# Kernel optimization log

Hardware: AMD Instinct MI355X
Metric: run time of the kernel (lower is better)

The kernel has to match this reference:

```python
import jax, jax.numpy as jnp
import numpy as np
from jax import lax

H = 32  # hidden size


def _lstm_layer(x, Wih, Whh, bih, bhh):
    """x: [B, T, D_in]; returns [B, T, H]. PyTorch gate order i,f,g,o."""
    B = x.shape[0]
    b = bih + bhh  # [4H]
    # precompute input projections for all timesteps: [T, B, 4H]
    xp = jnp.einsum('btd,gd->tbg', x, Wih) + b

    def step(carry, xt):
        h, c = carry
        gates = xt + h @ Whh.T  # [B, 4H]
        i, f, g, o = jnp.split(gates, 4, axis=-1)
        i = jax.nn.sigmoid(i)
        f = jax.nn.sigmoid(f)
        g = jnp.tanh(g)
        o = jax.nn.sigmoid(o)
        c = f * c + i * g
        h = o * jnp.tanh(c)
        return (h, c), h

    init = (jnp.zeros((B, H), x.dtype), jnp.zeros((B, H), x.dtype))
    _, ys = lax.scan(step, init, xp)  # ys: [T, B, H]
    return jnp.swapaxes(ys, 0, 1)


def _lstm5(x, Wih0, Wih_rest, Whh, bih, bhh):
    h = _lstm_layer(x, Wih0, Whh[0], bih[0], bhh[0])
    for l in range(4):  # fixed small layer count
        h = _lstm_layer(h, Wih_rest[l], Whh[l + 1], bih[l + 1], bhh[l + 1])
    return h


def setup_inputs() -> dict:
    key = jax.random.key(0)
    ks = jax.random.split(key, 18)
    s = 1.0 / np.sqrt(H)
    B, T = 16384, 20
    u = lambda k, shp: jax.random.uniform(k, shp, jnp.float32, -s, s)
    return {
        'accel': jax.random.normal(ks[0], (B, T, 3), jnp.float32),
        'gyro': jax.random.normal(ks[1], (B, T, 3), jnp.float32),
        'accel_Wih0': u(ks[2], (4 * H, 3)),
        'accel_Wih_rest': u(ks[3], (4, 4 * H, H)),
        'accel_Whh': u(ks[4], (5, 4 * H, H)),
        'accel_bih': u(ks[5], (5, 4 * H)),
        'accel_bhh': u(ks[6], (5, 4 * H)),
        'gyro_Wih0': u(ks[7], (4 * H, 3)),
        'gyro_Wih_rest': u(ks[8], (4, 4 * H, H)),
        'gyro_Whh': u(ks[9], (5, 4 * H, H)),
        'gyro_bih': u(ks[10], (5, 4 * H)),
        'gyro_bhh': u(ks[11], (5, 4 * H)),
        'fc1_w': u(ks[12], (128, T * H * 2)),
        'fc1_b': u(ks[13], (128,)),
        'fc2_w': u(ks[14], (5, 128)),
        'fc2_b': u(ks[15], (5,)),
    }


def reference(accel, gyro, accel_Wih0, accel_Wih_rest, accel_Whh, accel_bih,
              accel_bhh, gyro_Wih0, gyro_Wih_rest, gyro_Whh, gyro_bih,
              gyro_bhh, fc1_w, fc1_b, fc2_w, fc2_b):
    a = _lstm5(accel, accel_Wih0, accel_Wih_rest, accel_Whh, accel_bih, accel_bhh)
    g = _lstm5(gyro, gyro_Wih0, gyro_Wih_rest, gyro_Whh, gyro_bih, gyro_bhh)
    x = jnp.concatenate([a, g], axis=1)          # [B, 2T, H]
    x = x.reshape(x.shape[0], -1)                # [B, 2*T*H]
    x = jax.nn.relu(x @ fc1_w.T + fc1_b)         # [B, 128]
    return x @ fc2_w.T + fc2_b                   # [B, 5]
```

## Files before the change

kernel.cpp:

```cpp
#include <hip/hip_runtime.h>
#include <math.h>

#define B_TOTAL 16384
#define T_STEPS 20
#define NGRP    1024

typedef __attribute__((ext_vector_type(8))) __bf16 bf16x8;
typedef __attribute__((ext_vector_type(4))) float f32x4;

#define LOG2E_F 1.4426950408889634f
#define K2_F    2.8853900817779268f

__device__ __forceinline__ float exp2_fast(float x) {
#if __has_builtin(__builtin_amdgcn_exp2f)
    return __builtin_amdgcn_exp2f(x);
#else
    return __expf(x * 0.6931471805599453f);
#endif
}

__device__ __forceinline__ __bf16 bf16_bits(unsigned short s) {
    __bf16 r; __builtin_memcpy(&r, &s, 2); return r;
}
__device__ __forceinline__ void split_trunc(float x, __bf16& hi, __bf16& lo) {
    unsigned u = __float_as_uint(x);
    hi = bf16_bits((unsigned short)(u >> 16));
    float l = x - __uint_as_float(u & 0xFFFF0000u);
    lo = bf16_bits((unsigned short)(__float_as_uint(l) >> 16));
}

__device__ __forceinline__ float lstm_act2(f32x4 a, float& c) {
    float eA = exp2_fast(-a[0]);
    float eB = exp2_fast(-a[1]);
    float eC = exp2_fast(a[2]);
    float aA = 1.0f + eA, aB = 1.0f + eB, aC = 1.0f + eC;
    float pAC = aA * aC;
    float r1  = __builtin_amdgcn_rcpf(pAC * aB);
    c = fmaf(c, pAC, (eC - 1.0f) * aB) * r1;
    float eD = exp2_fast(-a[3]);
    float eE = exp2_fast(K2_F * c);
    float r2 = __builtin_amdgcn_rcpf((1.0f + eD) * (1.0f + eE));
    return (eE - 1.0f) * r2;
}

__global__ __launch_bounds__(512, 8)
void lstm5_mfma(const float* __restrict__ accel, const float* __restrict__ gyro,
                const float* __restrict__ aWih0, const float* __restrict__ aWihR,
                const float* __restrict__ aWhh,  const float* __restrict__ aBih,
                const float* __restrict__ aBhh,
                const float* __restrict__ gWih0, const float* __restrict__ gWihR,
                const float* __restrict__ gWhh,  const float* __restrict__ gBih,
                const float* __restrict__ gBhh,
                __bf16* __restrict__ Xhi, __bf16* __restrict__ Xlo) {
    const int tid  = threadIdx.x;
    const int w    = tid >> 6;
    const int lane = tid & 63;
    const int e    = lane & 15;
    const int quad = lane >> 4;
    const int sensor = blockIdx.y;
    const int bbase  = blockIdx.x * 16;

    const float* xin  = sensor ? gyro  : accel;
    const float* Wih0 = sensor ? gWih0 : aWih0;
    const float* WihR = sensor ? gWihR : aWihR;
    const float* Whh  = sensor ? gWhh  : aWhh;
    const float* Bih  = sensor ? gBih  : aBih;
    const float* Bhh  = sensor ? gBhh  : aBhh;

    __shared__ __align__(16) __bf16 shi[T_STEPS * 512];
    __shared__ __align__(16) __bf16 slo[T_STEPS * 512];

    const int ug  = w * 4 + quad;
    const int swz = (e >> 1) & 3;

    const int widx = (e * 16 + ((w * 2 + (quad >> 1)) ^ (swz << 2))) * 2 + (quad & 1);
    const int rb_base = e * 32 + ((quad ^ swz) << 3);

    const int m_row = lane & 15;
    const int orow  = (m_row & 3) * 32 + (w * 4 + (m_row >> 2));
    const float wscale = ((m_row & 3) == 2) ? K2_F : LOG2E_F;

    bf16x8 wih_h, wih_l, whh_h, whh_l;
    bf16x8 ih_h, ih_l;
    f32x4  biasv;
    float  c0 = 0.f;

#define LOAD_FRAG(Wsrc, fh, fl)                               \
    {                                                         \
        const float* p_ = (Wsrc) + (orow) * 32 + quad * 8;    \
        _Pragma("unroll")                                     \
        for (int jj = 0; jj < 8; ++jj) {                      \
            __bf16 h_, l_;                                    \
            split_trunc(p_[jj] * wscale, h_, l_);             \
            (fh)[jj] = h_;  (fl)[jj] = l_;                    \
        }                                                     \
    }

#define LOAD_BIAS(l)                                                        \
    {                                                                       \
        _Pragma("unroll")                                                   \
        for (int r = 0; r < 4; ++r) {                                       \
            float bs_ = (r == 2) ? K2_F : LOG2E_F;                          \
            biasv[r] = (Bih[(l) * 128 + r * 32 + ug] +                      \
                        Bhh[(l) * 128 + r * 32 + ug]) * bs_;                \
        }                                                                   \
    }

    {
        LOAD_FRAG(Whh, whh_h, whh_l);
        LOAD_BIAS(0);
        float w0reg[4][3];
#pragma unroll
        for (int r = 0; r < 4; ++r) {
            float bs_ = (r == 2) ? K2_F : LOG2E_F;
#pragma unroll
            for (int k = 0; k < 3; ++k)
                w0reg[r][k] = Wih0[(r * 32 + ug) * 3 + k] * bs_;
        }
        const float* xrow = xin + (size_t)(bbase + e) * (T_STEPS * 3);

        for (int t = 0; t < T_STEPS; ++t) {
            float x0 = xrow[t * 3 + 0];
            float x1 = xrow[t * 3 + 1];
            float x2 = xrow[t * 3 + 2];
            f32x4 acc = biasv;
#pragma unroll
            for (int r = 0; r < 4; ++r)
                acc[r] = fmaf(w0reg[r][0], x0,
                         fmaf(w0reg[r][1], x1,
                         fmaf(w0reg[r][2], x2, acc[r])));
            if (t > 0) {
                int rb = (t - 1) * 512 + rb_base;
                bf16x8 bh = *(const bf16x8*)&shi[rb];
                bf16x8 bl = *(const bf16x8*)&slo[rb];
                acc = __builtin_amdgcn_mfma_f32_16x16x32_bf16(whh_h, bh, acc, 0, 0, 0);
                acc = __builtin_amdgcn_mfma_f32_16x16x32_bf16(whh_h, bl, acc, 0, 0, 0);
                acc = __builtin_amdgcn_mfma_f32_16x16x32_bf16(whh_l, bh, acc, 0, 0, 0);
            }
            float h0 = lstm_act2(acc, c0);
            __bf16 hh_, ll_;
            split_trunc(h0, hh_, ll_);
            shi[t * 512 + widx] = hh_;
            slo[t * 512 + widx] = ll_;
            __syncthreads();
        }
    }

#define STEP_L(t)                                                           \
    {                                                                       \
        bf16x8 bh, bl, pf_h, pf_l;                                          \
        if ((t) > 0) {                                                      \
            bh = *(const bf16x8*)&shi[((t) - 1) * 512 + rb_base];           \
            bl = *(const bf16x8*)&slo[((t) - 1) * 512 + rb_base];           \
        }                                                                   \
        if ((t) < T_STEPS - 1) {               \
            pf_h = *(const bf16x8*)&shi[((t) + 1) * 512 + rb_base];         \
            pf_l = *(const bf16x8*)&slo[((t) + 1) * 512 + rb_base];         \
        }                                                                   \
        f32x4 acc;                                                          \
        acc = __builtin_amdgcn_mfma_f32_16x16x32_bf16(wih_h, ih_h, biasv, 0, 0, 0); \
        acc = __builtin_amdgcn_mfma_f32_16x16x32_bf16(wih_h, ih_l, acc, 0, 0, 0);   \
        acc = __builtin_amdgcn_mfma_f32_16x16x32_bf16(wih_l, ih_h, acc, 0, 0, 0);   \
        if ((t) > 0) {                                                      \
            acc = __builtin_amdgcn_mfma_f32_16x16x32_bf16(whh_h, bh, acc, 0, 0, 0); \
            acc = __builtin_amdgcn_mfma_f32_16x16x32_bf16(whh_h, bl, acc, 0, 0, 0); \
            acc = __builtin_amdgcn_mfma_f32_16x16x32_bf16(whh_l, bh, acc, 0, 0, 0); \
        }                                                                   \
        float h0 = lstm_act2(acc, c0);                                      \
        __bf16 hh_, ll_;                                                    \
        split_trunc(h0, hh_, ll_);                                          \
        shi[(t) * 512 + widx] = hh_;                                        \
        slo[(t) * 512 + widx] = ll_;                                        \
        if ((t) < T_STEPS - 1) { ih_h = pf_h; ih_l = pf_l; }                \
        __syncthreads();                 \
    }

    for (int l = 1; l < 5; ++l) {
        const float* Wi = WihR + (l - 1) * 4096;
        const float* Wh = Whh + l * 4096;
        LOAD_FRAG(Wi, wih_h, wih_l);
        LOAD_FRAG(Wh, whh_h, whh_l);
        LOAD_BIAS(l);
        c0 = 0.f;

        ih_h = *(const bf16x8*)&shi[rb_base];
        ih_l = *(const bf16x8*)&slo[rb_base];
        __syncthreads();

#pragma unroll
        for (int t = 0; t < T_STEPS; ++t) STEP_L(t);
    }
    __syncthreads();

    {
        size_t base = ((size_t)(sensor * NGRP + blockIdx.x)) * (20 * 512);
        float4* dh = (float4*)(Xhi + base);
        float4* dl = (float4*)(Xlo + base);
        const float4* sh = (const float4*)shi;
        const float4* sl = (const float4*)slo;
        for (int i = tid; i < 1280; i += 512) { dh[i] = sh[i]; dl[i] = sl[i]; }
    }
#undef LOAD_FRAG
#undef LOAD_BIAS
#undef STEP_L
}

__global__ void w1_prep(const float* __restrict__ w1,
                        __bf16* __restrict__ w1ah, __bf16* __restrict__ w1al) {
    int t = blockIdx.x * blockDim.x + threadIdx.x;
    if (t >= 20480) return;
    int lane = t & 63;
    int ks   = (t >> 6) % 40;
    int mt   = t / (64 * 40);
    int row  = mt * 16 + (lane & 15);
    int col0 = ks * 32 + (lane >> 4) * 8;
    const float* src = w1 + row * 1280 + col0;
#pragma unroll
    for (int j = 0; j < 8; ++j) {
        __bf16 h_, l_;
        split_trunc(src[j], h_, l_);
        w1ah[t * 8 + j] = h_;
        w1al[t * 8 + j] = l_;
    }
}

__global__ __launch_bounds__(256, 4)
void fc_mfma(const __bf16* __restrict__ Xhi, const __bf16* __restrict__ Xlo,
             const __bf16* __restrict__ w1ah, const __bf16* __restrict__ w1al,
             const float* __restrict__ fc1_b, const float* __restrict__ fc2_w,
             const float* __restrict__ fc2_b, float* __restrict__ out) {
    const int tid  = threadIdx.x;
    const int wv   = tid >> 6;
    const int lane = tid & 63;
    const int e    = lane & 15;
    const int quad = lane >> 4;
    const int g    = blockIdx.x;

    const int lnoff = e * 32 + ((quad ^ ((e >> 1) & 3)) << 3);

    __shared__ __align__(16) f32x4 sacc[4][8][64];
    __shared__ float sred[4][16][5];

    f32x4 acc[8];
#pragma unroll
    for (int m = 0; m < 8; ++m) acc[m] = (f32x4){0.f, 0.f, 0.f, 0.f};

    for (int kk = 0; kk < 10; ++kk) {
        int ks = wv * 10 + kk;
        int sensor = ks / 20, t = ks % 20;
        size_t bb = ((size_t)(sensor * NGRP + g)) * (20 * 512) + t * 512 + lnoff;
        bf16x8 bh = *(const bf16x8*)(Xhi + bb);
        bf16x8 bl = *(const bf16x8*)(Xlo + bb);
#pragma unroll
        for (int m = 0; m < 8; ++m) {
            const __bf16* ap = w1ah + ((size_t)((m * 40 + ks) * 64 + lane)) * 8;
            const __bf16* al = w1al + ((size_t)((m * 40 + ks) * 64 + lane)) * 8;
            bf16x8 ah = *(const bf16x8*)ap;
            bf16x8 av = *(const bf16x8*)al;
            acc[m] = __builtin_amdgcn_mfma_f32_16x16x32_bf16(ah, bh, acc[m], 0, 0, 0);
            acc[m] = __builtin_amdgcn_mfma_f32_16x16x32_bf16(ah, bl, acc[m], 0, 0, 0);
            acc[m] = __builtin_amdgcn_mfma_f32_16x16x32_bf16(av, bh, acc[m], 0, 0, 0);
        }
    }
#pragma unroll
    for (int m = 0; m < 8; ++m) sacc[wv][m][lane] = acc[m];
    __syncthreads();

    float p[5] = {0.f, 0.f, 0.f, 0.f, 0.f};
#pragma unroll
    for (int mm = 0; mm < 2; ++mm) {
        int mt = wv * 2 + mm;
        f32x4 z = sacc[0][mt][lane];
#pragma unroll
        for (int k = 1; k < 4; ++k) {
            f32x4 zz = sacc[k][mt][lane];
#pragma unroll
            for (int r = 0; r < 4; ++r) z[r] += zz[r];
        }
#pragma unroll
        for (int r = 0; r < 4; ++r) {
            int row = mt * 16 + quad * 4 + r;
            float v = fmaxf(z[r] + fc1_b[row], 0.f);
#pragma unroll
            for (int n = 0; n < 5; ++n) p[n] = fmaf(v, fc2_w[n * 128 + row], p[n]);
        }
    }
#pragma unroll
    for (int n = 0; n < 5; ++n) {
        p[n] += __shfl_xor(p[n], 16, 64);
        p[n] += __shfl_xor(p[n], 32, 64);
    }
    if (quad == 0) {
#pragma unroll
        for (int n = 0; n < 5; ++n) sred[wv][e][n] = p[n];
    }
    __syncthreads();
    if (tid < 80) {
        int col = tid / 5, n = tid - col * 5;
        out[(size_t)(g * 16 + col) * 5 + n] =
            sred[0][col][n] + sred[1][col][n] + sred[2][col][n] + sred[3][col][n] + fc2_b[n];
    }
}

extern "C" void kernel_launch(void* const* d_in, const int* in_sizes, int n_in,
                              void* d_out, int out_size, void* d_ws, size_t ws_size,
                              hipStream_t stream) {
    const float* accel  = (const float*)d_in[0];
    const float* gyro   = (const float*)d_in[1];
    const float* aWih0  = (const float*)d_in[2];
    const float* aWihR  = (const float*)d_in[3];
    const float* aWhh   = (const float*)d_in[4];
    const float* aBih   = (const float*)d_in[5];
    const float* aBhh   = (const float*)d_in[6];
    const float* gWih0  = (const float*)d_in[7];
    const float* gWihR  = (const float*)d_in[8];
    const float* gWhh   = (const float*)d_in[9];
    const float* gBih   = (const float*)d_in[10];
    const float* gBhh   = (const float*)d_in[11];
    const float* fc1_w  = (const float*)d_in[12];
    const float* fc1_b  = (const float*)d_in[13];
    const float* fc2_w  = (const float*)d_in[14];
    const float* fc2_b  = (const float*)d_in[15];
    float* out = (float*)d_out;

    const size_t XN = (size_t)2 * NGRP * 20 * 512;
    __bf16* Xhi  = (__bf16*)d_ws;
    __bf16* Xlo  = Xhi + XN;
    __bf16* W1ah = Xlo + XN;
    __bf16* W1al = W1ah + 163840;

    hipLaunchKernelGGL(w1_prep, dim3(80), dim3(256), 0, stream, fc1_w, W1ah, W1al);

    hipLaunchKernelGGL(lstm5_mfma, dim3(NGRP, 2), dim3(512), 0, stream,
                       accel, gyro, aWih0, aWihR, aWhh, aBih, aBhh,
                       gWih0, gWihR, gWhh, gBih, gBhh, Xhi, Xlo);

    hipLaunchKernelGGL(fc_mfma, dim3(NGRP), dim3(256), 0, stream,
                       Xhi, Xlo, W1ah, W1al, fc1_b, fc2_w, fc2_b, out);
}
```

Baseline: 285.7 us.

## Fuse fc1 GEMM into LSTM kernel epilogue, emit per-sensor partial sums

The LSTM kernel now runs the fc1 matmul directly from its shared-memory hidden states. Each wave computes one 16-row tile of the 128 outputs over its sensor's 20 timesteps and writes fp32 partial sums. This removes the round trip through global memory of the bf16 hi/lo hidden-state buffers, and a small reduce kernel now adds the two sensor partials and applies ReLU and fc2. In exchange, the LSTM kernel does extra MFMA work and global weight loads in its tail, and the removed __syncthreads before the shared-memory reads needs the last step to already be synchronised.

```diff
diff --git a/kernel.cpp b/kernel.cpp
--- a/kernel.cpp
+++ b/kernel.cpp
@@ -51,7 +51,8 @@
                 const float* __restrict__ gWih0, const float* __restrict__ gWihR,
                 const float* __restrict__ gWhh,  const float* __restrict__ gBih,
                 const float* __restrict__ gBhh,
-                __bf16* __restrict__ Xhi, __bf16* __restrict__ Xlo) {
+                const __bf16* __restrict__ w1ah, const __bf16* __restrict__ w1al,
+                float* __restrict__ partial) {
     const int tid  = threadIdx.x;
     const int w    = tid >> 6;
     const int lane = tid & 63;
@@ -190,15 +191,25 @@
 #pragma unroll
         for (int t = 0; t < T_STEPS; ++t) STEP_L(t);
     }
-    __syncthreads();
 
     {
-        size_t base = ((size_t)(sensor * NGRP + blockIdx.x)) * (20 * 512);
-        float4* dh = (float4*)(Xhi + base);
-        float4* dl = (float4*)(Xlo + base);
-        const float4* sh = (const float4*)shi;
-        const float4* sl = (const float4*)slo;
-        for (int i = tid; i < 1280; i += 512) { dh[i] = sh[i]; dl[i] = sl[i]; }
+        const __bf16* Wh1 = w1ah + ((size_t)(w * 40 + sensor * 20) * 64 + lane) * 8;
+        const __bf16* Wl1 = w1al + ((size_t)(w * 40 + sensor * 20) * 64 + lane) * 8;
+        f32x4 acc = (f32x4){0.f, 0.f, 0.f, 0.f};
+#pragma unroll
+        for (int t = 0; t < T_STEPS; ++t) {
+            bf16x8 bh = *(const bf16x8*)&shi[t * 512 + rb_base];
+            bf16x8 bl = *(const bf16x8*)&slo[t * 512 + rb_base];
+            bf16x8 ah = *(const bf16x8*)(Wh1 + (size_t)t * 512);
+            bf16x8 av = *(const bf16x8*)(Wl1 + (size_t)t * 512);
+            acc = __builtin_amdgcn_mfma_f32_16x16x32_bf16(ah, bh, acc, 0, 0, 0);
+            acc = __builtin_amdgcn_mfma_f32_16x16x32_bf16(ah, bl, acc, 0, 0, 0);
+            acc = __builtin_amdgcn_mfma_f32_16x16x32_bf16(av, bh, acc, 0, 0, 0);
+        }
+        float4 v = make_float4(acc[0], acc[1], acc[2], acc[3]);
+        *(float4*)(partial +
+                   ((size_t)(sensor * NGRP + blockIdx.x) * 8 + w) * 256 +
+                   e * 16 + quad * 4) = v;
     }
 #undef LOAD_FRAG
 #undef LOAD_BIAS
@@ -225,80 +236,46 @@
 }
 
 __global__ __launch_bounds__(256, 4)
-void fc_mfma(const __bf16* __restrict__ Xhi, const __bf16* __restrict__ Xlo,
-             const __bf16* __restrict__ w1ah, const __bf16* __restrict__ w1al,
-             const float* __restrict__ fc1_b, const float* __restrict__ fc2_w,
-             const float* __restrict__ fc2_b, float* __restrict__ out) {
-    const int tid  = threadIdx.x;
-    const int wv   = tid >> 6;
-    const int lane = tid & 63;
-    const int e    = lane & 15;
-    const int quad = lane >> 4;
-    const int g    = blockIdx.x;
-
-    const int lnoff = e * 32 + ((quad ^ ((e >> 1) & 3)) << 3);
-
-    __shared__ __align__(16) f32x4 sacc[4][8][64];
-    __shared__ float sred[4][16][5];
-
-    f32x4 acc[8];
-#pragma unroll
-    for (int m = 0; m < 8; ++m) acc[m] = (f32x4){0.f, 0.f, 0.f, 0.f};
-
-    for (int kk = 0; kk < 10; ++kk) {
-        int ks = wv * 10 + kk;
-        int sensor = ks / 20, t = ks % 20;
-        size_t bb = ((size_t)(sensor * NGRP + g)) * (20 * 512) + t * 512 + lnoff;
-        bf16x8 bh = *(const bf16x8*)(Xhi + bb);
-        bf16x8 bl = *(const bf16x8*)(Xlo + bb);
-#pragma unroll
-        for (int m = 0; m < 8; ++m) {
-            const __bf16* ap = w1ah + ((size_t)((m * 40 + ks) * 64 + lane)) * 8;
-            const __bf16* al = w1al + ((size_t)((m * 40 + ks) * 64 + lane)) * 8;
-            bf16x8 ah = *(const bf16x8*)ap;
-            bf16x8 av = *(const bf16x8*)al;
-            acc[m] = __builtin_amdgcn_mfma_f32_16x16x32_bf16(ah, bh, acc[m], 0, 0, 0);
-            acc[m] = __builtin_amdgcn_mfma_f32_16x16x32_bf16(ah, bl, acc[m], 0, 0, 0);
-            acc[m] = __builtin_amdgcn_mfma_f32_16x16x32_bf16(av, bh, acc[m], 0, 0, 0);
-        }
-    }
-#pragma unroll
-    for (int m = 0; m < 8; ++m) sacc[wv][m][lane] = acc[m];
-    __syncthreads();
+void fc2_reduce(const float* __restrict__ partial,
+                const float* __restrict__ fc1_b, const float* __restrict__ fc2_w,
+                const float* __restrict__ fc2_b, float* __restrict__ out) {
+    const int tid = threadIdx.x;
+    const int col = tid >> 4;
+    const int rg  = tid & 15;
+    const int g   = blockIdx.x;
+
+    const int row0 = rg * 8;
+    const int mt   = row0 >> 4;
+    const int rl0  = row0 & 15;
+    const float* pa = partial + ((size_t)g * 8 + mt) * 256 + col * 16 + rl0;
+    const float* pb = partial + ((size_t)(NGRP + g) * 8 + mt) * 256 + col * 16 + rl0;
+
+    float4 a0 = *(const float4*)(pa);
+    float4 a1 = *(const float4*)(pa + 4);
+    float4 b0 = *(const float4*)(pb);
+    float4 b1 = *(const float4*)(pb + 4);
+    float z[8] = {a0.x + b0.x, a0.y + b0.y, a0.z + b0.z, a0.w + b0.w,
+                  a1.x + b1.x, a1.y + b1.y, a1.z + b1.z, a1.w + b1.w};
 
     float p[5] = {0.f, 0.f, 0.f, 0.f, 0.f};
 #pragma unroll
-    for (int mm = 0; mm < 2; ++mm) {
-        int mt = wv * 2 + mm;
-        f32x4 z = sacc[0][mt][lane];
-#pragma unroll
-        for (int k = 1; k < 4; ++k) {
-            f32x4 zz = sacc[k][mt][lane];
-#pragma unroll
-            for (int r = 0; r < 4; ++r) z[r] += zz[r];
-        }
-#pragma unroll
-        for (int r = 0; r < 4; ++r) {
-            int row = mt * 16 + quad * 4 + r;
-            float v = fmaxf(z[r] + fc1_b[row], 0.f);
-#pragma unroll
-            for (int n = 0; n < 5; ++n) p[n] = fmaf(v, fc2_w[n * 128 + row], p[n]);
-        }
+    for (int rr = 0; rr < 8; ++rr) {
+        int row = row0 + rr;
+        float v = fmaxf(z[rr] + fc1_b[row], 0.f);
+#pragma unroll
+        for (int n = 0; n < 5; ++n) p[n] = fmaf(v, fc2_w[n * 128 + row], p[n]);
     }
 #pragma unroll
     for (int n = 0; n < 5; ++n) {
-        p[n] += __shfl_xor(p[n], 16, 64);
-        p[n] += __shfl_xor(p[n], 32, 64);
-    }
-    if (quad == 0) {
-#pragma unroll
-        for (int n = 0; n < 5; ++n) sred[wv][e][n] = p[n];
-    }
-    __syncthreads();
-    if (tid < 80) {
-        int col = tid / 5, n = tid - col * 5;
-        out[(size_t)(g * 16 + col) * 5 + n] =
-            sred[0][col][n] + sred[1][col][n] + sred[2][col][n] + sred[3][col][n] + fc2_b[n];
+        p[n] += __shfl_xor(p[n], 1, 64);
+        p[n] += __shfl_xor(p[n], 2, 64);
+        p[n] += __shfl_xor(p[n], 4, 64);
+        p[n] += __shfl_xor(p[n], 8, 64);
+    }
+    if (rg == 0) {
+#pragma unroll
+        for (int n = 0; n < 5; ++n)
+            out[((size_t)g * 16 + col) * 5 + n] = p[n] + fc2_b[n];
     }
 }
 
@@ -323,18 +300,16 @@
     const float* fc2_b  = (const float*)d_in[15];
     float* out = (float*)d_out;
 
-    const size_t XN = (size_t)2 * NGRP * 20 * 512;
-    __bf16* Xhi  = (__bf16*)d_ws;
-    __bf16* Xlo  = Xhi + XN;
-    __bf16* W1ah = Xlo + XN;
+    __bf16* W1ah = (__bf16*)d_ws;
     __bf16* W1al = W1ah + 163840;
+    float*  Pacc = (float*)(W1al + 163840);
 
     hipLaunchKernelGGL(w1_prep, dim3(80), dim3(256), 0, stream, fc1_w, W1ah, W1al);
 
     hipLaunchKernelGGL(lstm5_mfma, dim3(NGRP, 2), dim3(512), 0, stream,
                        accel, gyro, aWih0, aWihR, aWhh, aBih, aBhh,
-                       gWih0, gWihR, gWhh, gBih, gBhh, Xhi, Xlo);
-
-    hipLaunchKernelGGL(fc_mfma, dim3(NGRP), dim3(256), 0, stream,
-                       Xhi, Xlo, W1ah, W1al, fc1_b, fc2_w, fc2_b, out);
-}
+                       gWih0, gWihR, gWhh, gBih, gBhh, W1ah, W1al, Pacc);
+
+    hipLaunchKernelGGL(fc2_reduce, dim3(NGRP), dim3(256), 0, stream,
+                       Pacc, fc1_b, fc2_w, fc2_b, out);
+}
```

New measurement: 277.8 us. 1.03x faster.
